# Kernel optimization log

Measured on AMD Instinct MI355X. Metric: run time of the kernel, lower is better.

Reference implementation:

```python
import jax, jax.numpy as jnp
from jax import lax
import numpy as np

N, H, E, K = 8192, 1024, 8, 2


def setup_inputs() -> dict:
    key = jax.random.key(0)
    ks = jax.random.split(key, 6)
    s = 0.02
    return {
        "tokens": jax.random.normal(ks[0], (N, H), dtype=jnp.float32),
        "router_w": jax.random.normal(ks[1], (E, H), dtype=jnp.float32) * s,   # Linear(H,E,bias=False) weight [out,in]
        "w1": jax.random.normal(ks[2], (E, 2 * H, H), dtype=jnp.float32) * s,  # stacked expert fc1 [out,in]
        "b1": jax.random.normal(ks[3], (E, 2 * H), dtype=jnp.float32) * s,
        "w2": jax.random.normal(ks[4], (E, H, 2 * H), dtype=jnp.float32) * s,  # stacked expert fc2
        "b2": jax.random.normal(ks[5], (E, H), dtype=jnp.float32) * s,
    }


def reference(tokens, router_w, w1, b1, w2, b2):
    # Router logits and top-k dispatch weights
    logits = tokens @ router_w.T                      # [N, E]
    scores, idx = lax.top_k(logits, K)                # [N, K]
    probs = jax.nn.softmax(scores, axis=-1)           # softmax over the top-k scores only
    # combine[n, e] = prob if expert e selected for token n else 0
    combine = jnp.zeros((N, E), dtype=tokens.dtype)
    combine = combine.at[jnp.arange(N)[:, None], idx].add(probs)
    # Per-expert MLP (loop over fixed small E; zero combine weight masks non-selected)
    out = jnp.zeros_like(tokens)
    for e in range(E):
        h = jax.nn.gelu(tokens @ w1[e].T + b1[e], approximate=False)  # [N, 2H]
        y = h @ w2[e].T + b2[e]                                       # [N, H]
        out = out + combine[:, e:e + 1] * y
    return out
```

## Files before the change

kernel.cpp:

```cpp
#include <hip/hip_runtime.h>
#include <stdint.h>

#define N_TOK 8192
#define HDIM  1024
#define NEXP  8
#define CAP   16384
#define MAXTILE 136

typedef __bf16 bf16x8 __attribute__((ext_vector_type(8)));
typedef float  f32x4  __attribute__((ext_vector_type(4)));

__device__ inline unsigned short f2bf(float f) {
  union { float f; unsigned u; } v; v.f = f;
  return (unsigned short)((v.u + 0x7fffu + ((v.u >> 16) & 1u)) >> 16);
}

__device__ inline float bf2f(unsigned short b) {
  union { unsigned u; float f; } v; v.u = (unsigned)b << 16; return v.f;
}

__device__ inline float gelu_f(float x) {
  float y = 0.7978845608028654f * (x + 0.044715f * x * x * x);
  y = fminf(fmaxf(y, -15.f), 15.f);
  float t = __expf(2.f * y);
  return 0.5f * x * (1.f + (t - 1.f) / (t + 1.f));
}

__device__ inline void gld_lds16(const void* gptr, void* lptr) {
  __builtin_amdgcn_global_load_lds(
      (const __attribute__((address_space(1))) void*)(uintptr_t)gptr,
      (__attribute__((address_space(3))) void*)(uintptr_t)lptr,
      16, 0, 0);
}

__global__ __launch_bounds__(256) void cvt2_kernel(
    const float* __restrict__ s1, unsigned short* __restrict__ d1, int n1,
    const float* __restrict__ s2, unsigned short* __restrict__ d2, int n2) {
  int i = blockIdx.x * 256 + threadIdx.x;
  int stride = gridDim.x * 256;
  for (; i < n1 + n2; i += stride) {
    const float4* sp; ushort4* dp; int k;
    if (i < n1) { sp = (const float4*)s1; dp = (ushort4*)d1; k = i; }
    else        { sp = (const float4*)s2; dp = (ushort4*)d2; k = i - n1; }
    float4 v = sp[k];
    ushort4 o;
    o.x = f2bf(v.x); o.y = f2bf(v.y); o.z = f2bf(v.z); o.w = f2bf(v.w);
    dp[k] = o;
  }
}

__global__ __launch_bounds__(256) void router_kernel(
    const float* __restrict__ tokens, const float* __restrict__ rw,
    unsigned short* __restrict__ tokb, int* __restrict__ pair,
    float* __restrict__ probs) {
  int wid = threadIdx.x >> 6, lane = threadIdx.x & 63;
  int n = blockIdx.x * 4 + wid;
  const float4* trow = (const float4*)(tokens + (size_t)n * HDIM);
  ushort4* tdst = (ushort4*)(tokb + (size_t)n * HDIM);
  float acc[NEXP];
#pragma unroll
  for (int e = 0; e < NEXP; e++) acc[e] = 0.f;
#pragma unroll
  for (int it = 0; it < 4; it++) {
    int c4 = it * 64 + lane;
    float4 tv = trow[c4];
    ushort4 o;
    o.x = f2bf(tv.x); o.y = f2bf(tv.y); o.z = f2bf(tv.z); o.w = f2bf(tv.w);
    tdst[c4] = o;
#pragma unroll
    for (int e = 0; e < NEXP; e++) {
      float4 w = ((const float4*)(rw + e * HDIM))[c4];
      acc[e] += tv.x * w.x + tv.y * w.y + tv.z * w.z + tv.w * w.w;
    }
  }
#pragma unroll
  for (int e = 0; e < NEXP; e++) {
#pragma unroll
    for (int off = 32; off > 0; off >>= 1) acc[e] += __shfl_xor(acc[e], off, 64);
  }
  if (lane == 0) {
    int e0 = 0; float s0 = acc[0];
#pragma unroll
    for (int e = 1; e < NEXP; e++) if (acc[e] > s0) { s0 = acc[e]; e0 = e; }
    int e1 = -1; float s1 = -3.4e38f;
#pragma unroll
    for (int e = 0; e < NEXP; e++) if (e != e0 && acc[e] > s1) { s1 = acc[e]; e1 = e; }
    float z  = expf(s1 - s0);
    float p0 = 1.f / (1.f + z);
    pair[n] = e0 | (e1 << 8);
    probs[2 * n]     = p0;
    probs[2 * n + 1] = z * p0;
  }
}

__global__ __launch_bounds__(1024) void dispatch_kernel(
    const int* __restrict__ pair, int* __restrict__ counts,
    int* __restrict__ rowids) {
  int e = blockIdx.x;
  int t = threadIdx.x;
  __shared__ int sc[1024];
  int p8[8];
  int c = 0;
#pragma unroll
  for (int i = 0; i < 8; i++) {
    p8[i] = pair[t * 8 + i];
    c += ((p8[i] & 255) == e) + (((p8[i] >> 8) & 255) == e);
  }
  sc[t] = c;
  __syncthreads();
  for (int off = 1; off < 1024; off <<= 1) {
    int v = (t >= off) ? sc[t - off] : 0;
    __syncthreads();
    sc[t] += v;
    __syncthreads();
  }
  if (t == 1023) counts[e] = sc[1023];
  int* dst = rowids + e * CAP + (sc[t] - c);
#pragma unroll
  for (int i = 0; i < 8; i++) {
    int n = t * 8 + i;
    if ((p8[i] & 255) == e)        *dst++ = 2 * n;
    if (((p8[i] >> 8) & 255) == e) *dst++ = 2 * n + 1;
  }
}

__global__ void worklist_kernel(const int* __restrict__ counts, int* __restrict__ wl) {
  if (threadIdx.x == 0) {
    int p = 0;
    for (int e = 0; e < NEXP; e++) {
      int nt = (counts[e] + 127) >> 7;
      for (int i = 0; i < nt; i++) { wl[1 + p] = (e << 16) | i; p++; }
    }
    wl[0] = p;
  }
}

template <int MODE>
__global__ __launch_bounds__(1024) void moe_gemm(
    const unsigned short* __restrict__ Abase,
    const unsigned short* __restrict__ Wb,
    const float* __restrict__ bias,
    const int* __restrict__ counts, const int* __restrict__ rowids,
    const int* __restrict__ wl, const float* __restrict__ probs,
    unsigned short* __restrict__ dstbuf) {
  constexpr int KT   = MODE ? 32 : 16;
  constexpr int NCOL = MODE ? 1024 : 2048;
  constexpr int KDIM = MODE ? 2048 : 1024;

  int s = blockIdx.x & 7;
  int r = blockIdx.x >> 3;
  int tile, cb;
  if constexpr (MODE == 0) {
    tile = r >> 1;
    cb   = ((r & 1) << 3) + s;
  } else {
    tile = r;
    cb   = s;
  }
  if (tile >= wl[0]) return;
  int d  = wl[1 + tile];
  int e  = d >> 16;
  int rb = d & 0xffff;
  int ce = counts[e];
  const int* rl = rowids + e * CAP + rb * 128;

  int t = threadIdx.x;
  __shared__ __align__(16) char smem[65536];

  int jsrc = (t & 7) ^ ((t >> 3) & 7);
  int rr0 = t >> 3;
  int rid0 = (rb * 128 + rr0 < ce) ? rl[rr0] : rl[0];
  long arow = MODE ? (long)rid0 : (long)(rid0 >> 1);
  const char* asrc = (const char*)(Abase + arow * KDIM) + jsrc * 16;
  const char* bsrc = (const char*)(Wb + ((long)e * NCOL + cb * 128 + rr0) * KDIM) + jsrc * 16;

  auto stage = [&](int kt, char* buf) {
    gld_lds16(asrc + kt * 128, buf + t * 16);
    gld_lds16(bsrc + kt * 128, buf + 16384 + t * 16);
  };

  f32x4 acc[2][2];
#pragma unroll
  for (int mi = 0; mi < 2; mi++)
#pragma unroll
    for (int ni = 0; ni < 2; ni++) {
      f32x4 z = {0.f, 0.f, 0.f, 0.f};
      acc[mi][ni] = z;
    }

  int lane = t & 63, wid = t >> 6;
  int wr = wid >> 2, wc = wid & 3;
  int lr = lane >> 4, lc = lane & 15;

  stage(0, smem);
  stage(1, smem + 32768);

  for (int kt = 0; kt < KT; kt++) {
    if (kt + 1 < KT) {
      asm volatile("s_waitcnt vmcnt(2)" ::: "memory");
    } else {
      asm volatile("s_waitcnt vmcnt(0)" ::: "memory");
    }
    __builtin_amdgcn_s_barrier();
    __builtin_amdgcn_sched_barrier(0);
    char* cbuf = smem + ((kt & 1) << 15);
#pragma unroll
    for (int ks = 0; ks < 2; ks++) {
      bf16x8 af[2], bfv[2];
      int j = ks * 4 + lr;
#pragma unroll
      for (int mi = 0; mi < 2; mi++) {
        int rr = wr * 32 + mi * 16 + lc;
        af[mi] = *(const bf16x8*)(cbuf + rr * 128 + ((j ^ (rr & 7)) << 4));
      }
#pragma unroll
      for (int ni = 0; ni < 2; ni++) {
        int rr = wc * 32 + ni * 16 + lc;
        bfv[ni] = *(const bf16x8*)(cbuf + 16384 + rr * 128 + ((j ^ (rr & 7)) << 4));
      }
      __builtin_amdgcn_s_setprio(1);
#pragma unroll
      for (int mi = 0; mi < 2; mi++)
#pragma unroll
        for (int ni = 0; ni < 2; ni++)
          acc[mi][ni] = __builtin_amdgcn_mfma_f32_16x16x32_bf16(af[mi], bfv[ni], acc[mi][ni], 0, 0, 0);
      __builtin_amdgcn_s_setprio(0);
    }
    __builtin_amdgcn_s_barrier();
    __builtin_amdgcn_sched_barrier(0);
    if (kt + 2 < KT) stage(kt + 2, cbuf);
  }

  float bcol[2];
#pragma unroll
  for (int ni = 0; ni < 2; ni++)
    bcol[ni] = bias[e * NCOL + cb * 128 + wc * 32 + ni * 16 + lc];

#pragma unroll
  for (int mi = 0; mi < 2; mi++) {
#pragma unroll
    for (int r4 = 0; r4 < 4; r4++) {
      int lrow = wr * 32 + mi * 16 + lr * 4 + r4;
      float p = 1.f;
      if constexpr (MODE == 1)
        p = (rb * 128 + lrow < ce) ? probs[rl[lrow]] : 0.f;
#pragma unroll
      for (int ni = 0; ni < 2; ni++) {
        int col = wc * 32 + ni * 16 + lc;
        float x = acc[mi][ni][r4] + bcol[ni];
        if constexpr (MODE == 0)
          x = gelu_f(x);
        else
          x *= p;
        int j = col >> 3;
        *(unsigned short*)(smem + lrow * 256 + ((j ^ (lrow & 15)) << 4) + (col & 7) * 2) = f2bf(x);
      }
    }
  }
  __syncthreads();

  int row = t >> 3, q = t & 7;
  if (rb * 128 + row < ce) {
    int rid = rl[row];
    char* dst = (char*)(dstbuf + (long)rid * NCOL + cb * 128) + q * 32;
#pragma unroll
    for (int i = 0; i < 2; i++) {
      int j = q * 2 + i;
      *(int4*)(dst + i * 16) = *(const int4*)(smem + row * 256 + ((j ^ (row & 15)) << 4));
    }
  }
}

typedef short short8v __attribute__((ext_vector_type(8)));
__global__ __launch_bounds__(256) void merge_kernel(const unsigned short* __restrict__ Y,
                                                    float* __restrict__ out) {
  int i = blockIdx.x * 256 + threadIdx.x;
  int n = i >> 7, c = (i & 127) * 8;
  const short8v a = *(const short8v*)(Y + (long)(2 * n) * HDIM + c);
  const short8v b = *(const short8v*)(Y + (long)(2 * n + 1) * HDIM + c);
  float4 o0, o1;
#pragma unroll
  for (int k = 0; k < 8; k++) {
    float v = bf2f((unsigned short)a[k]) + bf2f((unsigned short)b[k]);
    if (k < 4) (&o0.x)[k] = v; else (&o1.x)[k - 4] = v;
  }
  float4* dst = (float4*)(out + (long)n * HDIM + c);
  dst[0] = o0; dst[1] = o1;
}

extern "C" void kernel_launch(void* const* d_in, const int* in_sizes, int n_in,
                              void* d_out, int out_size, void* d_ws, size_t ws_size,
                              hipStream_t stream) {
  const float* tokens   = (const float*)d_in[0];
  const float* router_w = (const float*)d_in[1];
  const float* w1       = (const float*)d_in[2];
  const float* b1       = (const float*)d_in[3];
  const float* w2       = (const float*)d_in[4];
  const float* b2       = (const float*)d_in[5];
  float* out = (float*)d_out;

  char* ws = (char*)d_ws;
  int*            counts = (int*)ws;
  int*            rowids = (int*)(ws + 64);
  float*          probs  = (float*)(ws + 64 + NEXP * CAP * 4);
  int*            pair   = (int*)(ws + 64 + NEXP * CAP * 4 + N_TOK * 2 * 4);
  int*            wl     = (int*)(ws + 64 + NEXP * CAP * 4 + N_TOK * 2 * 4 + N_TOK * 4);
  unsigned short* tokb   = (unsigned short*)(ws + (1u << 20));
  unsigned short* w1b    = (unsigned short*)(ws + (1u << 20) + 16777216u);
  unsigned short* w2b    = (unsigned short*)(ws + (1u << 20) + 16777216u + 33554432u);
  unsigned short* Hbuf   = (unsigned short*)(ws + (1u << 20) + 16777216u + 67108864u);
  unsigned short* Ybuf   = w1b;

  cvt2_kernel<<<4096, 256, 0, stream>>>(w1, w1b, NEXP * 2048 * 1024 / 4,
                                        w2, w2b, NEXP * 1024 * 2048 / 4);
  router_kernel<<<N_TOK / 4, 256, 0, stream>>>(tokens, router_w, tokb, pair, probs);
  dispatch_kernel<<<NEXP, 1024, 0, stream>>>(pair, counts, rowids);
  worklist_kernel<<<1, 64, 0, stream>>>(counts, wl);
  moe_gemm<0><<<MAXTILE * 16, 1024, 0, stream>>>(tokb, w1b, b1, counts, rowids, wl, probs, Hbuf);
  moe_gemm<1><<<MAXTILE * 8, 1024, 0, stream>>>(Hbuf, w2b, b2, counts, rowids, wl, probs, Ybuf);
  merge_kernel<<<N_TOK * HDIM / 8 / 256, 256, 0, stream>>>(Ybuf, out);
}
```

Before: 285.9 us.

## Partition MoE GEMM work into per-role worklists for cache-local scheduling

```diff
diff --git a/kernel.cpp b/kernel.cpp
--- a/kernel.cpp
+++ b/kernel.cpp
@@ -5,7 +5,8 @@
 #define HDIM  1024
 #define NEXP  8
 #define CAP   16384
-#define MAXTILE 136
+#define S0    320
+#define S1    192
 
 typedef __bf16 bf16x8 __attribute__((ext_vector_type(8)));
 typedef float  f32x4  __attribute__((ext_vector_type(4)));
@@ -124,14 +125,33 @@
   }
 }
 
-__global__ void worklist_kernel(const int* __restrict__ counts, int* __restrict__ wl) {
-  if (threadIdx.x == 0) {
+__global__ void worklist_kernel(const int* __restrict__ counts,
+                                int* __restrict__ wlb0, int* __restrict__ cnt0,
+                                int* __restrict__ wlb1, int* __restrict__ cnt1) {
+  int r = threadIdx.x;
+  if (r < 8) {
+    int h = r >> 2, q = r & 3;
     int p = 0;
     for (int e = 0; e < NEXP; e++) {
       int nt = (counts[e] + 127) >> 7;
-      for (int i = 0; i < nt; i++) { wl[1 + p] = (e << 16) | i; p++; }
-    }
-    wl[0] = p;
+      int h0 = (nt + 1) >> 1;
+      int t0 = h ? h0 : 0, t1 = h ? nt : h0;
+      for (int ti = t0; ti < t1; ti++)
+        for (int c = 0; c < 4; c++)
+          wlb0[r * S0 + p++] = (e << 24) | (ti << 8) | (q * 4 + c);
+    }
+    cnt0[r] = p;
+
+    int tq = r >> 1, cp = r & 1;
+    p = 0;
+    for (int e = 0; e < NEXP; e++) {
+      int nt = (counts[e] + 127) >> 7;
+      int b0 = (nt * tq) >> 2, b1 = (nt * (tq + 1)) >> 2;
+      for (int ti = b0; ti < b1; ti++)
+        for (int c = 0; c < 4; c++)
+          wlb1[r * S1 + p++] = (e << 24) | (ti << 8) | (cp * 4 + c);
+    }
+    cnt1[r] = p;
   }
 }
 
@@ -141,26 +161,21 @@
     const unsigned short* __restrict__ Wb,
     const float* __restrict__ bias,
     const int* __restrict__ counts, const int* __restrict__ rowids,
-    const int* __restrict__ wl, const float* __restrict__ probs,
+    const int* __restrict__ wlb, const int* __restrict__ cnt,
+    const float* __restrict__ probs,
     unsigned short* __restrict__ dstbuf) {
-  constexpr int KT   = MODE ? 32 : 16;
-  constexpr int NCOL = MODE ? 1024 : 2048;
-  constexpr int KDIM = MODE ? 2048 : 1024;
-
-  int s = blockIdx.x & 7;
-  int r = blockIdx.x >> 3;
-  int tile, cb;
-  if constexpr (MODE == 0) {
-    tile = r >> 1;
-    cb   = ((r & 1) << 3) + s;
-  } else {
-    tile = r;
-    cb   = s;
-  }
-  if (tile >= wl[0]) return;
-  int d  = wl[1 + tile];
-  int e  = d >> 16;
-  int rb = d & 0xffff;
+  constexpr int KT     = MODE ? 32 : 16;
+  constexpr int NCOL   = MODE ? 1024 : 2048;
+  constexpr int KDIM   = MODE ? 2048 : 1024;
+  constexpr int STRIDE = MODE ? S1 : S0;
+
+  int role = blockIdx.x & 7;
+  int j    = blockIdx.x >> 3;
+  if (j >= cnt[role]) return;
+  int desc = wlb[role * STRIDE + j];
+  int e  = desc >> 24;
+  int rb = (desc >> 8) & 0xffff;
+  int cb = desc & 255;
   int ce = counts[e];
   const int* rl = rowids + e * CAP + rb * 128;
 
@@ -207,16 +222,16 @@
 #pragma unroll
     for (int ks = 0; ks < 2; ks++) {
       bf16x8 af[2], bfv[2];
-      int j = ks * 4 + lr;
+      int jj = ks * 4 + lr;
 #pragma unroll
       for (int mi = 0; mi < 2; mi++) {
         int rr = wr * 32 + mi * 16 + lc;
-        af[mi] = *(const bf16x8*)(cbuf + rr * 128 + ((j ^ (rr & 7)) << 4));
+        af[mi] = *(const bf16x8*)(cbuf + rr * 128 + ((jj ^ (rr & 7)) << 4));
       }
 #pragma unroll
       for (int ni = 0; ni < 2; ni++) {
         int rr = wc * 32 + ni * 16 + lc;
-        bfv[ni] = *(const bf16x8*)(cbuf + 16384 + rr * 128 + ((j ^ (rr & 7)) << 4));
+        bfv[ni] = *(const bf16x8*)(cbuf + 16384 + rr * 128 + ((jj ^ (rr & 7)) << 4));
       }
       __builtin_amdgcn_s_setprio(1);
 #pragma unroll
@@ -252,8 +267,8 @@
           x = gelu_f(x);
         else
           x *= p;
-        int j = col >> 3;
-        *(unsigned short*)(smem + lrow * 256 + ((j ^ (lrow & 15)) << 4) + (col & 7) * 2) = f2bf(x);
+        int jc = col >> 3;
+        *(unsigned short*)(smem + lrow * 256 + ((jc ^ (lrow & 15)) << 4) + (col & 7) * 2) = f2bf(x);
       }
     }
   }
@@ -265,8 +280,8 @@
     char* dst = (char*)(dstbuf + (long)rid * NCOL + cb * 128) + q * 32;
 #pragma unroll
     for (int i = 0; i < 2; i++) {
-      int j = q * 2 + i;
-      *(int4*)(dst + i * 16) = *(const int4*)(smem + row * 256 + ((j ^ (row & 15)) << 4));
+      int jc = q * 2 + i;
+      *(int4*)(dst + i * 16) = *(const int4*)(smem + row * 256 + ((jc ^ (row & 15)) << 4));
     }
   }
 }
@@ -304,7 +319,11 @@
   int*            rowids = (int*)(ws + 64);
   float*          probs  = (float*)(ws + 64 + NEXP * CAP * 4);
   int*            pair   = (int*)(ws + 64 + NEXP * CAP * 4 + N_TOK * 2 * 4);
-  int*            wl     = (int*)(ws + 64 + NEXP * CAP * 4 + N_TOK * 2 * 4 + N_TOK * 4);
+  char*           wlbase = ws + 64 + NEXP * CAP * 4 + N_TOK * 2 * 4 + N_TOK * 4;
+  int*            cnt0   = (int*)wlbase;
+  int*            cnt1   = (int*)(wlbase + 64);
+  int*            wlb0   = (int*)(wlbase + 128);
+  int*            wlb1   = (int*)(wlbase + 128 + 8 * S0 * 4);
   unsigned short* tokb   = (unsigned short*)(ws + (1u << 20));
   unsigned short* w1b    = (unsigned short*)(ws + (1u << 20) + 16777216u);
   unsigned short* w2b    = (unsigned short*)(ws + (1u << 20) + 16777216u + 33554432u);
@@ -315,8 +334,8 @@
                                         w2, w2b, NEXP * 1024 * 2048 / 4);
   router_kernel<<<N_TOK / 4, 256, 0, stream>>>(tokens, router_w, tokb, pair, probs);
   dispatch_kernel<<<NEXP, 1024, 0, stream>>>(pair, counts, rowids);
-  worklist_kernel<<<1, 64, 0, stream>>>(counts, wl);
-  moe_gemm<0><<<MAXTILE * 16, 1024, 0, stream>>>(tokb, w1b, b1, counts, rowids, wl, probs, Hbuf);
-  moe_gemm<1><<<MAXTILE * 8, 1024, 0, stream>>>(Hbuf, w2b, b2, counts, rowids, wl, probs, Ybuf);
+  worklist_kernel<<<1, 64, 0, stream>>>(counts, wlb0, cnt0, wlb1, cnt1);
+  moe_gemm<0><<<8 * S0, 1024, 0, stream>>>(tokb, w1b, b1, counts, rowids, wlb0, cnt0, probs, Hbuf);
+  moe_gemm<1><<<8 * S1, 1024, 0, stream>>>(Hbuf, w2b, b2, counts, rowids, wlb1, cnt1, probs, Ybuf);
   merge_kernel<<<N_TOK * HDIM / 8 / 256, 256, 0, stream>>>(Ybuf, out);
 }
```

New measurement: 274.2 us (median of 2 runs). 4.1% less time.
